# Optimization experiments

Hardware: AMD Instinct MI355X
Metric: run time of the kernel (lower is better)

The kernel has to match this reference:

```python
import jax, jax.numpy as jnp
import numpy as np

T, D, H = 10, 45, 45  # time steps, input features, hidden size (hard-coded in source)


def _lstm_step(x, h, c, W_ih, W_hh, b_ih, b_hh):
    # PyTorch nn.LSTM single step; gate order i, f, g, o
    gates = x @ W_ih.T + b_ih + h @ W_hh.T + b_hh
    i, f, g, o = jnp.split(gates, 4, axis=-1)
    c2 = jax.nn.sigmoid(f) * c + jax.nn.sigmoid(i) * jnp.tanh(g)
    h2 = jax.nn.sigmoid(o) * jnp.tanh(c2)
    return h2, c2


def setup_inputs() -> dict:
    key = jax.random.key(0)
    ks = jax.random.split(key, 20)
    s = 0.1
    return {
        "price_input": jax.random.normal(ks[0], (T, D), dtype=jnp.float32),
        # encoder input attention: Linear(2H+T -> 1)
        "Wa": jax.random.normal(ks[1], (1, 2 * H + T), dtype=jnp.float32) * s,
        "ba": jax.random.normal(ks[2], (1,), dtype=jnp.float32) * s,
        # encoder LSTM
        "Wih_e": jax.random.normal(ks[3], (4 * H, D), dtype=jnp.float32) * s,
        "Whh_e": jax.random.normal(ks[4], (4 * H, H), dtype=jnp.float32) * s,
        "bih_e": jax.random.normal(ks[5], (4 * H,), dtype=jnp.float32) * s,
        "bhh_e": jax.random.normal(ks[6], (4 * H,), dtype=jnp.float32) * s,
        # decoder temporal attention: Linear(2H+D -> D), Tanh, Linear(D -> 1)
        "W1": jax.random.normal(ks[7], (D, 2 * H + D), dtype=jnp.float32) * s,
        "b1": jax.random.normal(ks[8], (D,), dtype=jnp.float32) * s,
        "W2": jax.random.normal(ks[9], (1, D), dtype=jnp.float32) * s,
        "b2": jax.random.normal(ks[10], (1,), dtype=jnp.float32) * s,
        # decoder LSTM (input dim = D)
        "Wih_d": jax.random.normal(ks[11], (4 * H, D), dtype=jnp.float32) * s,
        "Whh_d": jax.random.normal(ks[12], (4 * H, H), dtype=jnp.float32) * s,
        "bih_d": jax.random.normal(ks[13], (4 * H,), dtype=jnp.float32) * s,
        "bhh_d": jax.random.normal(ks[14], (4 * H,), dtype=jnp.float32) * s,
        # final fc: Linear(2H -> predict_size=45)
        "Wfc": jax.random.normal(ks[15], (45, 2 * H), dtype=jnp.float32) * s,
        "bfc": jax.random.normal(ks[16], (45,), dtype=jnp.float32) * s,
    }


def reference(price_input, Wa, ba, Wih_e, Whh_e, bih_e, bhh_e,
              W1, b1, W2, b2, Wih_d, Whh_d, bih_d, bhh_d, Wfc, bfc):
    x = price_input[None]                      # [1, T, D]
    xT = jnp.transpose(x, (0, 2, 1))           # [1, D, T]

    def enc_step(carry, x_t):
        h, c = carry                           # each [1, H]
        hr = jnp.broadcast_to(h[:, None, :], (1, D, H))
        cr = jnp.broadcast_to(c[:, None, :], (1, D, H))
        feat = jnp.concatenate([hr, cr, xT], axis=2)      # [1, D, 2H+T]
        scores = (feat @ Wa.T + ba)[..., 0]               # [1, D]
        attn = jax.nn.softmax(scores, axis=-1)            # over input features
        wi = attn * x_t[None]                             # [1, D]
        h2, c2 = _lstm_step(wi, h, c, Wih_e, Whh_e, bih_e, bhh_e)
        return (h2, c2), h2

    z = jnp.zeros((1, H), dtype=price_input.dtype)
    (_, _), hs = jax.lax.scan(enc_step, (z, z), price_input)
    price_vec = jnp.transpose(hs, (1, 0, 2))              # [1, T, H]

    # decoder: temporal attention over the T encoder states (hidden=cell=0)
    h0 = jnp.zeros((1, H), dtype=price_input.dtype)
    c0 = h0
    hr = jnp.broadcast_to(h0[:, None, :], (1, T, H))
    feat = jnp.concatenate([hr, hr, price_vec], axis=2)   # [1, T, 2H+D]
    scores = (jnp.tanh(feat @ W1.T + b1) @ W2.T + b2)[..., 0]  # [1, T]
    attn = jax.nn.softmax(scores, axis=-1)
    context = jnp.einsum('bt,bth->bh', attn, price_vec)   # [1, H]

    h1, _ = _lstm_step(context, h0, c0, Wih_d, Whh_d, bih_d, bhh_d)
    y_pred = jnp.concatenate([h1, context], axis=1) @ Wfc.T + bfc  # [1, 45]
    return y_pred
```

## Files before the change

### kernel.cpp

```cpp
#include <hip/hip_runtime.h>


static constexpr int NT = 10;
static constexpr int ND = 45;
static constexpr int NH = 45;
static constexpr int NG = 4 * NH;

__device__ __forceinline__ float sigf(float x) {
    return 1.0f / (1.0f + __expf(-x));
}

__global__ __launch_bounds__(256) void darnn_kernel(
    const float* __restrict__ X,
    const float* __restrict__ Wa,
    const float* __restrict__ Wih_e,
    const float* __restrict__ Whh_e,
    const float* __restrict__ bih_e,
    const float* __restrict__ bhh_e,
    const float* __restrict__ W1,
    const float* __restrict__ b1,
    const float* __restrict__ W2,
    const float* __restrict__ Wih_d,
    const float* __restrict__ bih_d,
    const float* __restrict__ bhh_d,
    const float* __restrict__ Wfc,
    const float* __restrict__ bfc,
    float* __restrict__ out)
{
    const int tid = threadIdx.x;

    __shared__ float sX[NT * ND];
    __shared__ float sWi[NT * ND];
    __shared__ float sWhh[NG * NH];
    __shared__ float sGx[NT * NG];
    __shared__ float sh[NH], sc[NH];
    __shared__ float sgates[NG];
    __shared__ float shs[NT * NH];
    __shared__ float sattn[ND];
    __shared__ float sdec[NT * NH];
    __shared__ float sat[NT];
    __shared__ float sctx[NH];
    __shared__ float sh1[NH];

    for (int i = tid; i < NT * ND; i += 256) sX[i] = X[i];
    for (int i = tid; i < NG * NH; i += 256) sWhh[i] = Whh_e[i];
    if (tid < NH) { sh[tid] = 0.0f; sc[tid] = 0.0f; }
    __syncthreads();

    if (tid < 64) {
        float acc = -1e30f;
        if (tid < ND) {
            acc = 0.0f;
            for (int t = 0; t < NT; ++t) acc += Wa[90 + t] * sX[t * ND + tid];
        }
        float m = acc;
        for (int off = 32; off; off >>= 1) m = fmaxf(m, __shfl_xor(m, off, 64));
        float e = (tid < ND) ? __expf(acc - m) : 0.0f;
        float s = e;
        for (int off = 32; off; off >>= 1) s += __shfl_xor(s, off, 64);
        if (tid < ND) sattn[tid] = e / s;
    }
    __syncthreads();

    for (int i = tid; i < NT * ND; i += 256) sWi[i] = sattn[i % ND] * sX[i];
    __syncthreads();

    for (int i = tid; i < NT * NG; i += 256) {
        const int t = i / NG, g = i % NG;
        const float* __restrict__ wr = Wih_e + g * ND;
        const float* wi = sWi + t * ND;
        float a0 = bih_e[g] + bhh_e[g], a1 = 0.f, a2 = 0.f, a3 = 0.f;
        int d = 0;
        for (; d + 3 < ND; d += 4) {
            a0 += wr[d]     * wi[d];
            a1 += wr[d + 1] * wi[d + 1];
            a2 += wr[d + 2] * wi[d + 2];
            a3 += wr[d + 3] * wi[d + 3];
        }
        for (; d < ND; ++d) a0 += wr[d] * wi[d];
        sGx[i] = (a0 + a1) + (a2 + a3);
    }
    __syncthreads();

    for (int t = 0; t < NT; ++t) {
        if (tid < NG) {
            const float* wr = sWhh + tid * NH;
            float a0 = sGx[t * NG + tid], a1 = 0.f, a2 = 0.f, a3 = 0.f;
            int k = 0;
            for (; k + 3 < NH; k += 4) {
                a0 += wr[k]     * sh[k];
                a1 += wr[k + 1] * sh[k + 1];
                a2 += wr[k + 2] * sh[k + 2];
                a3 += wr[k + 3] * sh[k + 3];
            }
            for (; k < NH; ++k) a0 += wr[k] * sh[k];
            sgates[tid] = (a0 + a1) + (a2 + a3);
        }
        __syncthreads();
        if (tid < NH) {
            float ig = sigf(sgates[tid]);
            float fg = sigf(sgates[NH + tid]);
            float gg = tanhf(sgates[2 * NH + tid]);
            float og = sigf(sgates[3 * NH + tid]);
            float c2 = fg * sc[tid] + ig * gg;
            float h2 = og * tanhf(c2);
            sc[tid] = c2;
            sh[tid] = h2;
            shs[t * NH + tid] = h2;
        }
        __syncthreads();
    }

    for (int i = tid; i < NT * NH; i += 256) {
        const int t = i / NH, k = i % NH;
        const float* __restrict__ wr = W1 + k * (2 * NH + ND) + 2 * NH;
        const float* hv = shs + t * NH;
        float a0 = b1[k], a1 = 0.f, a2 = 0.f, a3 = 0.f;
        int j = 0;
        for (; j + 3 < ND; j += 4) {
            a0 += wr[j]     * hv[j];
            a1 += wr[j + 1] * hv[j + 1];
            a2 += wr[j + 2] * hv[j + 2];
            a3 += wr[j + 3] * hv[j + 3];
        }
        for (; j < ND; ++j) a0 += wr[j] * hv[j];
        sdec[i] = W2[k] * tanhf((a0 + a1) + (a2 + a3));
    }
    __syncthreads();

    if (tid < NT) {
        float acc = 0.0f;
        for (int k = 0; k < NH; ++k) acc += sdec[tid * NH + k];
        sat[tid] = acc;
    }
    __syncthreads();
    if (tid == 0) {
        float m = -1e30f;
        for (int t = 0; t < NT; ++t) m = fmaxf(m, sat[t]);
        float e[NT], s = 0.0f;
        for (int t = 0; t < NT; ++t) { e[t] = __expf(sat[t] - m); s += e[t]; }
        float inv = 1.0f / s;
        for (int t = 0; t < NT; ++t) sat[t] = e[t] * inv;
    }
    __syncthreads();

    if (tid < NH) {
        float acc = 0.0f;
        for (int t = 0; t < NT; ++t) acc += sat[t] * shs[t * NH + tid];
        sctx[tid] = acc;
    }
    __syncthreads();

    if (tid < NG) {
        const float* __restrict__ wr = Wih_d + tid * ND;
        float a0 = bih_d[tid] + bhh_d[tid], a1 = 0.f, a2 = 0.f, a3 = 0.f;
        int d = 0;
        for (; d + 3 < ND; d += 4) {
            a0 += wr[d]     * sctx[d];
            a1 += wr[d + 1] * sctx[d + 1];
            a2 += wr[d + 2] * sctx[d + 2];
            a3 += wr[d + 3] * sctx[d + 3];
        }
        for (; d < ND; ++d) a0 += wr[d] * sctx[d];
        sgates[tid] = (a0 + a1) + (a2 + a3);
    }
    __syncthreads();
    if (tid < NH) {
        float ig = sigf(sgates[tid]);
        float gg = tanhf(sgates[2 * NH + tid]);
        float og = sigf(sgates[3 * NH + tid]);
        float c2 = ig * gg;
        sh1[tid] = og * tanhf(c2);
    }
    __syncthreads();

    if (tid < 45) {
        const float* __restrict__ wr = Wfc + tid * (2 * NH);
        float a0 = bfc[tid], a1 = 0.f;
        for (int j = 0; j < NH; ++j) {
            a0 += wr[j]      * sh1[j];
            a1 += wr[NH + j] * sctx[j];
        }
        out[tid] = a0 + a1;
    }
}

extern "C" void kernel_launch(void* const* d_in, const int* in_sizes, int n_in,
                              void* d_out, int out_size, void* d_ws, size_t ws_size,
                              hipStream_t stream) {
    const float* X     = (const float*)d_in[0];
    const float* Wa    = (const float*)d_in[1];
    const float* Wih_e = (const float*)d_in[3];
    const float* Whh_e = (const float*)d_in[4];
    const float* bih_e = (const float*)d_in[5];
    const float* bhh_e = (const float*)d_in[6];
    const float* W1    = (const float*)d_in[7];
    const float* b1    = (const float*)d_in[8];
    const float* W2    = (const float*)d_in[9];
    const float* Wih_d = (const float*)d_in[11];
    const float* bih_d = (const float*)d_in[13];
    const float* bhh_d = (const float*)d_in[14];
    const float* Wfc   = (const float*)d_in[15];
    const float* bfc   = (const float*)d_in[16];
    float* out = (float*)d_out;

    darnn_kernel<<<dim3(1), dim3(256), 0, stream>>>(
        X, Wa, Wih_e, Whh_e, bih_e, bhh_e, W1, b1, W2,
        Wih_d, bih_d, bhh_d, Wfc, bfc, out);
}
```

Measured before the change: 108.7 us.

## Run encoder LSTM recurrence in one wave with register weights, overlap weight staging

The encoder recurrence now runs on a single wavefront. Each lane keeps its four Whh rows in registers and broadcasts h through cross-lane shuffles, which removes the per-step block barriers and shared-memory round trips. While wave 0 runs the recurrence, the other waves preload the decoder Wih, Wfc and the W1 slice into registers or shared memory. The input-gate projection is reorganised so each thread computes all time steps for one gate. Fast rcp-based sigmoid and tanh replace tanhf and division, which slightly changes accuracy and adds heavy register pressure (180 weight floats per lane).

After: 104.7 us. 3.7% less time.

```diff
diff --git a/kernel.cpp b/kernel.cpp
--- a/kernel.cpp
+++ b/kernel.cpp
@@ -6,9 +6,9 @@
 static constexpr int NH = 45;
 static constexpr int NG = 4 * NH;
 
-__device__ __forceinline__ float sigf(float x) {
-    return 1.0f / (1.0f + __expf(-x));
-}
+__device__ __forceinline__ float rcp_(float x) { return __builtin_amdgcn_rcpf(x); }
+__device__ __forceinline__ float sigf(float x) { return rcp_(1.0f + __expf(-x)); }
+__device__ __forceinline__ float tanh_(float x) { return 1.0f - 2.0f * rcp_(1.0f + __expf(2.0f * x)); }
 
 __global__ __launch_bounds__(256) void darnn_kernel(
     const float* __restrict__ X,
@@ -27,111 +27,136 @@
     const float* __restrict__ bfc,
     float* __restrict__ out)
 {
-    const int tid = threadIdx.x;
+    const int tid  = threadIdx.x;
+    const int wave = tid >> 6;
+    const int lane = tid & 63;
 
     __shared__ float sX[NT * ND];
+    __shared__ float sattn[ND];
     __shared__ float sWi[NT * ND];
-    __shared__ float sWhh[NG * NH];
     __shared__ float sGx[NT * NG];
-    __shared__ float sh[NH], sc[NH];
-    __shared__ float sgates[NG];
     __shared__ float shs[NT * NH];
-    __shared__ float sattn[ND];
-    __shared__ float sdec[NT * NH];
+    __shared__ float sW1c[ND * ND];
+    __shared__ float sWfc[45 * 2 * NH];
+    __shared__ float sb1[ND];
+    __shared__ float sW2v[ND];
+    __shared__ float sbfcv[45];
     __shared__ float sat[NT];
     __shared__ float sctx[NH];
-    __shared__ float sh1[NH];
-
-    for (int i = tid; i < NT * ND; i += 256) sX[i] = X[i];
-    for (int i = tid; i < NG * NH; i += 256) sWhh[i] = Whh_e[i];
-    if (tid < NH) { sh[tid] = 0.0f; sc[tid] = 0.0f; }
-    __syncthreads();
-
-    if (tid < 64) {
+    __shared__ float sh1v[NH];
+    __shared__ float sg[NG];
+    __shared__ float sdec[NT * NH];
+
+    float w0[45], w1[45], w2[45], w3[45];
+    if (wave == 0) {
+        const int j = (lane < 45) ? lane : 0;
+        const float* r0 = Whh_e + (j)       * NH;
+        const float* r1 = Whh_e + (45 + j)  * NH;
+        const float* r2 = Whh_e + (90 + j)  * NH;
+        const float* r3 = Whh_e + (135 + j) * NH;
+#pragma unroll
+        for (int k = 0; k < 45; ++k) {
+            w0[k] = r0[k]; w1[k] = r1[k]; w2[k] = r2[k]; w3[k] = r3[k];
+        }
+    } else {
+        for (int i = tid - 64; i < NT * ND; i += 192) sX[i] = X[i];
+    }
+    __syncthreads();
+
+    if (wave == 1) {
+        const int l = lane;
         float acc = -1e30f;
-        if (tid < ND) {
+        if (l < ND) {
             acc = 0.0f;
-            for (int t = 0; t < NT; ++t) acc += Wa[90 + t] * sX[t * ND + tid];
+            for (int t = 0; t < NT; ++t) acc += Wa[90 + t] * sX[t * ND + l];
         }
         float m = acc;
         for (int off = 32; off; off >>= 1) m = fmaxf(m, __shfl_xor(m, off, 64));
-        float e = (tid < ND) ? __expf(acc - m) : 0.0f;
+        float e = (l < ND) ? __expf(acc - m) : 0.0f;
         float s = e;
         for (int off = 32; off; off >>= 1) s += __shfl_xor(s, off, 64);
-        if (tid < ND) sattn[tid] = e / s;
-    }
-    __syncthreads();
-
-    for (int i = tid; i < NT * ND; i += 256) sWi[i] = sattn[i % ND] * sX[i];
-    __syncthreads();
-
-    for (int i = tid; i < NT * NG; i += 256) {
-        const int t = i / NG, g = i % NG;
-        const float* __restrict__ wr = Wih_e + g * ND;
-        const float* wi = sWi + t * ND;
-        float a0 = bih_e[g] + bhh_e[g], a1 = 0.f, a2 = 0.f, a3 = 0.f;
-        int d = 0;
-        for (; d + 3 < ND; d += 4) {
-            a0 += wr[d]     * wi[d];
-            a1 += wr[d + 1] * wi[d + 1];
-            a2 += wr[d + 2] * wi[d + 2];
-            a3 += wr[d + 3] * wi[d + 3];
-        }
-        for (; d < ND; ++d) a0 += wr[d] * wi[d];
-        sGx[i] = (a0 + a1) + (a2 + a3);
-    }
-    __syncthreads();
-
-    for (int t = 0; t < NT; ++t) {
-        if (tid < NG) {
-            const float* wr = sWhh + tid * NH;
-            float a0 = sGx[t * NG + tid], a1 = 0.f, a2 = 0.f, a3 = 0.f;
-            int k = 0;
-            for (; k + 3 < NH; k += 4) {
-                a0 += wr[k]     * sh[k];
-                a1 += wr[k + 1] * sh[k + 1];
-                a2 += wr[k + 2] * sh[k + 2];
-                a3 += wr[k + 3] * sh[k + 3];
+        if (l < ND) sattn[l] = e * rcp_(s);
+    }
+    __syncthreads();
+
+    if (wave > 0)
+        for (int i = tid - 64; i < NT * ND; i += 192) sWi[i] = sattn[i % ND] * sX[i];
+    __syncthreads();
+
+    if (wave > 0) {
+        const int g = tid - 64;
+        if (g < NG) {
+            float acc[NT];
+            const float b = bih_e[g] + bhh_e[g];
+#pragma unroll
+            for (int t = 0; t < NT; ++t) acc[t] = b;
+            const float* wr = Wih_e + g * ND;
+            for (int d = 0; d < ND; ++d) {
+                const float wv = wr[d];
+#pragma unroll
+                for (int t = 0; t < NT; ++t) acc[t] += wv * sWi[t * ND + d];
             }
-            for (; k < NH; ++k) a0 += wr[k] * sh[k];
-            sgates[tid] = (a0 + a1) + (a2 + a3);
-        }
-        __syncthreads();
-        if (tid < NH) {
-            float ig = sigf(sgates[tid]);
-            float fg = sigf(sgates[NH + tid]);
-            float gg = tanhf(sgates[2 * NH + tid]);
-            float og = sigf(sgates[3 * NH + tid]);
-            float c2 = fg * sc[tid] + ig * gg;
-            float h2 = og * tanhf(c2);
-            sc[tid] = c2;
-            sh[tid] = h2;
-            shs[t * NH + tid] = h2;
-        }
-        __syncthreads();
-    }
+#pragma unroll
+            for (int t = 0; t < NT; ++t) sGx[t * NG + g] = acc[t];
+        }
+    }
+    __syncthreads();
+
+    float wd[45];
+    float bd = 0.0f;
+    if (wave == 0) {
+        const int j = (lane < 45) ? lane : 0;
+        float h = 0.0f, c = 0.0f;
+        for (int t = 0; t < NT; ++t) {
+            float a0 = sGx[t * NG + j];
+            float a1 = sGx[t * NG + 45 + j];
+            float a2 = sGx[t * NG + 90 + j];
+            float a3 = sGx[t * NG + 135 + j];
+#pragma unroll
+            for (int k = 0; k < 45; ++k) {
+                const float hk = __shfl(h, k, 64);
+                a0 += w0[k] * hk; a1 += w1[k] * hk;
+                a2 += w2[k] * hk; a3 += w3[k] * hk;
+            }
+            c = sigf(a1) * c + sigf(a0) * tanh_(a2);
+            h = sigf(a3) * tanh_(c);
+            if (lane < 45) shs[t * NH + lane] = h;
+        }
+    } else {
+        const int i0 = tid - 64;
+        if (i0 < NG) {
+            const float* wr = Wih_d + i0 * ND;
+#pragma unroll
+            for (int d = 0; d < 45; ++d) wd[d] = wr[d];
+            bd = bih_d[i0] + bhh_d[i0];
+        }
+        {
+            const float2* s = (const float2*)Wfc;
+            float2* d2 = (float2*)sWfc;
+            for (int i = i0; i < 2025; i += 192) d2[i] = s[i];
+        }
+        for (int i = i0; i < ND * ND; i += 192) {
+            const int r = i / 45, cc = i - r * 45;
+            sW1c[i] = W1[r * 135 + 90 + cc];
+        }
+        if (i0 < 45) { sb1[i0] = b1[i0]; sW2v[i0] = W2[i0]; sbfcv[i0] = bfc[i0]; }
+    }
+    __syncthreads();
 
     for (int i = tid; i < NT * NH; i += 256) {
-        const int t = i / NH, k = i % NH;
-        const float* __restrict__ wr = W1 + k * (2 * NH + ND) + 2 * NH;
+        const int t = i / NH, k = i - t * NH;
+        const float* wr = sW1c + k * ND;
         const float* hv = shs + t * NH;
-        float a0 = b1[k], a1 = 0.f, a2 = 0.f, a3 = 0.f;
-        int j = 0;
-        for (; j + 3 < ND; j += 4) {
-            a0 += wr[j]     * hv[j];
-            a1 += wr[j + 1] * hv[j + 1];
-            a2 += wr[j + 2] * hv[j + 2];
-            a3 += wr[j + 3] * hv[j + 3];
-        }
-        for (; j < ND; ++j) a0 += wr[j] * hv[j];
-        sdec[i] = W2[k] * tanhf((a0 + a1) + (a2 + a3));
+        float a = sb1[k];
+        for (int jj = 0; jj < ND; ++jj) a += wr[jj] * hv[jj];
+        sdec[i] = sW2v[k] * tanh_(a);
     }
     __syncthreads();
 
     if (tid < NT) {
-        float acc = 0.0f;
-        for (int k = 0; k < NH; ++k) acc += sdec[tid * NH + k];
-        sat[tid] = acc;
+        float a = 0.0f;
+        for (int k = 0; k < NH; ++k) a += sdec[tid * NH + k];
+        sat[tid] = a;
     }
     __syncthreads();
     if (tid == 0) {
@@ -139,49 +164,42 @@
         for (int t = 0; t < NT; ++t) m = fmaxf(m, sat[t]);
         float e[NT], s = 0.0f;
         for (int t = 0; t < NT; ++t) { e[t] = __expf(sat[t] - m); s += e[t]; }
-        float inv = 1.0f / s;
+        const float inv = rcp_(s);
         for (int t = 0; t < NT; ++t) sat[t] = e[t] * inv;
     }
     __syncthreads();
 
     if (tid < NH) {
-        float acc = 0.0f;
-        for (int t = 0; t < NT; ++t) acc += sat[t] * shs[t * NH + tid];
-        sctx[tid] = acc;
-    }
-    __syncthreads();
-
-    if (tid < NG) {
-        const float* __restrict__ wr = Wih_d + tid * ND;
-        float a0 = bih_d[tid] + bhh_d[tid], a1 = 0.f, a2 = 0.f, a3 = 0.f;
-        int d = 0;
-        for (; d + 3 < ND; d += 4) {
-            a0 += wr[d]     * sctx[d];
-            a1 += wr[d + 1] * sctx[d + 1];
-            a2 += wr[d + 2] * sctx[d + 2];
-            a3 += wr[d + 3] * sctx[d + 3];
-        }
-        for (; d < ND; ++d) a0 += wr[d] * sctx[d];
-        sgates[tid] = (a0 + a1) + (a2 + a3);
+        float a = 0.0f;
+        for (int t = 0; t < NT; ++t) a += sat[t] * shs[t * NH + tid];
+        sctx[tid] = a;
+    }
+    __syncthreads();
+
+    if (wave > 0) {
+        const int g = tid - 64;
+        if (g < NG) {
+            float a = bd;
+#pragma unroll
+            for (int d = 0; d < 45; ++d) a += wd[d] * sctx[d];
+            sg[g] = a;
+        }
     }
     __syncthreads();
     if (tid < NH) {
-        float ig = sigf(sgates[tid]);
-        float gg = tanhf(sgates[2 * NH + tid]);
-        float og = sigf(sgates[3 * NH + tid]);
-        float c2 = ig * gg;
-        sh1[tid] = og * tanhf(c2);
+        const float ig = sigf(sg[tid]);
+        const float gg = tanh_(sg[2 * NH + tid]);
+        const float og = sigf(sg[3 * NH + tid]);
+        sh1v[tid] = og * tanh_(ig * gg);
     }
     __syncthreads();
 
     if (tid < 45) {
-        const float* __restrict__ wr = Wfc + tid * (2 * NH);
-        float a0 = bfc[tid], a1 = 0.f;
-        for (int j = 0; j < NH; ++j) {
-            a0 += wr[j]      * sh1[j];
-            a1 += wr[NH + j] * sctx[j];
-        }
-        out[tid] = a0 + a1;
+        const float* wr = sWfc + tid * (2 * NH);
+        float a = sbfcv[tid];
+        for (int jj = 0; jj < NH; ++jj) a += wr[jj] * sh1v[jj];
+        for (int jj = 0; jj < NH; ++jj) a += wr[NH + jj] * sctx[jj];
+        out[tid] = a;
     }
 }
 
```
